# Optimization experiments

Hardware: AMD Instinct MI355X
Metric: run time of the kernel (lower is better)

## Reference

```python
import jax, jax.numpy as jnp
import numpy as np

N_DRUG, N_MICROBE = 1500, 1572
N = N_DRUG + N_MICROBE          # 3072 nodes
F_IN = 1546                     # raw feature dim (fc1: 1546 -> 256)
D0 = 256                        # GCN input dim after fc1
H1 = H2 = 128                   # GCN hidden dims (H1 + H2 = 256)
B = 16384                       # number of (left,right) query pairs


def _sym_norm(A):
    # D^{-1/2} A D^{-1/2} (no self loops), zeros kept for isolated nodes
    deg = A.sum(axis=1)
    d = jnp.where(deg > 0, jax.lax.rsqrt(deg), 0.0)
    return A * d[:, None] * d[None, :]


def _compute_inf(adj, L):
    # dl.compute_inf: L-hop influence = L-th power of sym-normalized adjacency
    An = _sym_norm(adj)
    M = An
    for _ in range(L - 1):
        M = M @ An
    return M


def _gcn_norm(W):
    # GCNConv normalization: add self loops (weight 1), sym-normalize by weighted degree
    Ahat = W + jnp.eye(W.shape[0], dtype=W.dtype)
    deg = Ahat.sum(axis=1)
    d = jnp.where(deg > 0, jax.lax.rsqrt(deg), 0.0)
    return Ahat * d[:, None] * d[None, :]


def _glorot(key, shape):
    return jax.random.normal(key, shape, dtype=jnp.float32) / np.sqrt(shape[0])


def setup_inputs() -> dict:
    key = jax.random.key(0)
    ks = jax.random.split(key, 24)
    u = jax.random.uniform(ks[0], (N, N), dtype=jnp.float32)
    w = jax.random.uniform(ks[1], (N, N), dtype=jnp.float32)
    adj = jnp.where(u < 0.01, w, 0.0)
    adj = jnp.maximum(adj, adj.T)
    X = jax.random.normal(ks[2], (N, F_IN), dtype=jnp.float32)
    left = jax.random.randint(ks[3], (B,), 0, N)
    right = jax.random.randint(ks[4], (B,), 0, N)
    return dict(
        left=left, right=right, X=X, adj=adj, threshold=jnp.float32(1e-4),
        W_fc1=_glorot(ks[5], (F_IN, D0)), b_fc1=jnp.zeros((D0,), jnp.float32),
        Wg1=_glorot(ks[6], (D0, H1)), bg1=jnp.zeros((H1,), jnp.float32),
        Wg2=_glorot(ks[7], (H1, H2)), bg2=jnp.zeros((H2,), jnp.float32),
        Wg3=_glorot(ks[8], (D0, H1)), bg3=jnp.zeros((H1,), jnp.float32),
        Wg4=_glorot(ks[9], (H1, H2)), bg4=jnp.zeros((H2,), jnp.float32),
        Wg5=_glorot(ks[10], (D0, H1)), bg5=jnp.zeros((H1,), jnp.float32),
        Wg6=_glorot(ks[11], (H1, H2)), bg6=jnp.zeros((H2,), jnp.float32),
        cnn_k=jax.random.normal(ks[12], (1, 3, 3, 3), dtype=jnp.float32) * 0.1,
        cnn_b=jnp.zeros((1,), jnp.float32),
        W_a=_glorot(ks[13], (2 * (H1 + H2), 64)), b_a=jnp.zeros((64,), jnp.float32),
        W_b=_glorot(ks[14], (64, 2)), b_b=jnp.zeros((2,), jnp.float32),
    )


def reference(left, right, X, adj, threshold,
              W_fc1, b_fc1, Wg1, bg1, Wg2, bg2, Wg3, bg3, Wg4, bg4,
              Wg5, bg5, Wg6, bg6, cnn_k, cnn_b, W_a, b_a, W_b, b_b):
    X0 = jax.nn.relu(X @ W_fc1 + b_fc1)  # fc1: [N, 1546] -> [N, 256]

    def branch(mask_src, Wa, ba, Wb, bb):
        # dynamically thresholded edges carry the ORIGINAL adj weights
        Wadj = jnp.where(mask_src > threshold, adj, 0.0)
        An = _gcn_norm(Wadj)                       # [N, N]
        e1 = jax.nn.relu(An @ (X0 @ Wa) + ba)      # GCNConv 1
        e2 = jax.nn.relu(An @ (e1 @ Wb) + bb)      # GCNConv 2
        return jnp.concatenate([e1, e2], axis=1)   # [N, 256]

    emb_l2 = branch(_compute_inf(adj, 2), Wg1, bg1, Wg2, bg2)
    emb_l1 = branch(_compute_inf(adj, 1), Wg3, bg3, Wg4, bg4)
    emb_l0 = branch(adj, Wg5, bg5, Wg6, bg6)

    emb = jnp.stack([emb_l0, emb_l1, emb_l2], axis=0)[None]  # [1, 3, N, 256]
    conv = jax.lax.conv_general_dilated(
        emb, cnn_k, window_strides=(1, 1), padding=[(2, 2), (2, 2)],
        rhs_dilation=(2, 2), dimension_numbers=('NCHW', 'OIHW', 'NCHW'))
    emb_all = conv[0, 0] + cnn_b[0]                # [N, 256]

    pair = jnp.concatenate([emb_all[left], emb_all[right]], axis=1)  # [B, 512]
    h = jax.nn.relu(pair @ W_a + b_a)              # dropout is identity at eval
    logits = h @ W_b + b_b                         # [B, 2]
    return logits, emb_all
```

## Files before the change

### kernel.cpp

```cpp
#include <hip/hip_runtime.h>

#define NN 3072
#define FIN 1546
#define KP 1568
#define MAXR 192

#define XS4_BLOCKS (NN * KP / 1024)
#define WSPLIT_BLOCKS (256 * KP / 256)
#define WG_BLOCKS 704
#define CSR_BLOCKS (NN / 4)
#define FC1_BLOCKS (NN / 16 * 4)

typedef __attribute__((ext_vector_type(8))) __bf16 bf16x8;
typedef __attribute__((ext_vector_type(4))) __bf16 bf16x4;
typedef __attribute__((ext_vector_type(4))) float f32x4;

__global__ __launch_bounds__(256) void prep_k(const float* __restrict__ adj,
                                              int* __restrict__ cols, float* __restrict__ vals,
                                              int* __restrict__ cnt, float* __restrict__ dvec,
                                              const float* __restrict__ X,
                                              __bf16* __restrict__ Xh, __bf16* __restrict__ Xl,
                                              const float* __restrict__ W,
                                              __bf16* __restrict__ WhT, __bf16* __restrict__ WlT,
                                              const float* __restrict__ Wga0,
                                              const float* __restrict__ Wga1,
                                              const float* __restrict__ Wga2,
                                              const float* __restrict__ Wgb0,
                                              const float* __restrict__ Wgb1,
                                              const float* __restrict__ Wgb2,
                                              const float* __restrict__ Wa,
                                              __bf16* __restrict__ WgaTh, __bf16* __restrict__ WgaTl,
                                              __bf16* __restrict__ WgbTh, __bf16* __restrict__ WgbTl,
                                              __bf16* __restrict__ WaTh, __bf16* __restrict__ WaTl) {
    int bid = blockIdx.x;
    if (bid < XS4_BLOCKS) {
        int e = (bid * 256 + threadIdx.x) * 4;
        int i = e / KP, c = e - i * KP;
        const float* xr = X + (size_t)i * FIN + c;
        float x0 = (c + 0 < FIN) ? xr[0] : 0.f;
        float x1 = (c + 1 < FIN) ? xr[1] : 0.f;
        float x2 = (c + 2 < FIN) ? xr[2] : 0.f;
        float x3 = (c + 3 < FIN) ? xr[3] : 0.f;
        __bf16 h0 = (__bf16)x0, h1 = (__bf16)x1, h2 = (__bf16)x2, h3 = (__bf16)x3;
        bf16x4 hv = {h0, h1, h2, h3};
        bf16x4 lv = {(__bf16)(x0 - (float)h0), (__bf16)(x1 - (float)h1),
                     (__bf16)(x2 - (float)h2), (__bf16)(x3 - (float)h3)};
        *(bf16x4*)(Xh + e) = hv;
        *(bf16x4*)(Xl + e) = lv;
        return;
    }
    bid -= XS4_BLOCKS;
    if (bid < WSPLIT_BLOCKS) {
        int idx = bid * 256 + threadIdx.x;
        int c = idx / KP, k = idx - c * KP;
        float x = (k < FIN) ? W[(size_t)k * 256 + c] : 0.f;
        __bf16 h = (__bf16)x;
        WhT[idx] = h;
        WlT[idx] = (__bf16)(x - (float)h);
        return;
    }
    bid -= WSPLIT_BLOCKS;
    if (bid < WG_BLOCKS) {
        int idx = bid * 256 + threadIdx.x;
        float x;
        __bf16 *oh, *ol;
        int off;
        if (idx < 98304) {
            int b = idx >> 15, r = idx & 32767;
            int c = r >> 8, k = r & 255;
            const float* Wp = (b == 0) ? Wga0 : (b == 1) ? Wga1 : Wga2;
            x = Wp[k * 128 + c];
            oh = WgaTh; ol = WgaTl; off = idx;
        } else if (idx < 98304 + 49152) {
            int j = idx - 98304;
            int b = j >> 14, r = j & 16383;
            int c = r >> 7, k = r & 127;
            const float* Wp = (b == 0) ? Wgb0 : (b == 1) ? Wgb1 : Wgb2;
            x = Wp[k * 128 + c];
            oh = WgbTh; ol = WgbTl; off = j;
        } else {
            int j = idx - 147456;
            int c = j >> 8, k = j & 255;
            x = (c < 64) ? Wa[(size_t)k * 64 + c] : Wa[(size_t)(256 + k) * 64 + (c - 64)];
            oh = WaTh; ol = WaTl; off = j;
        }
        __bf16 h = (__bf16)x;
        oh[off] = h;
        ol[off] = (__bf16)(x - (float)h);
        return;
    }
    bid -= WG_BLOCKS;
    int i = bid * 4 + (threadIdx.x >> 6);
    int lane = threadIdx.x & 63;
    const float* row = adj + (size_t)i * NN;
    unsigned long long below = (1ull << lane) - 1ull;
    float s = 0.f; int count = 0;
    int base = i * MAXR;
    for (int c0 = 0; c0 < NN; c0 += 256) {
        float4 a4 = *(const float4*)(row + c0 + lane * 4);
        float a[4] = {a4.x, a4.y, a4.z, a4.w};
        s += a[0] + a[1] + a[2] + a[3];
        unsigned long long bal[4];
        #pragma unroll
        for (int u = 0; u < 4; u++) bal[u] = __ballot(a[u] != 0.f);
        int before = 0;
        #pragma unroll
        for (int u = 0; u < 4; u++) before += __popcll(bal[u] & below);
        int local = 0;
        #pragma unroll
        for (int u = 0; u < 4; u++) {
            if (a[u] != 0.f) {
                int pos = count + before + local;
                if (pos < MAXR) { cols[base + pos] = c0 + lane * 4 + u; vals[base + pos] = a[u]; }
                local++;
            }
        }
        int tot = 0;
        #pragma unroll
        for (int u = 0; u < 4; u++) tot += __popcll(bal[u]);
        count += tot;
    }
    for (int off = 32; off; off >>= 1) s += __shfl_xor(s, off);
    if (lane == 0) {
        cnt[i] = count < MAXR ? count : MAXR;
        dvec[i] = (s > 0.f) ? 1.0f / sqrtf(s) : 0.f;
    }
}

__global__ __launch_bounds__(256) void fc1mask_k(const int* __restrict__ cols,
                                                 const float* __restrict__ vals,
                                                 const int* __restrict__ cnt,
                                                 const float* __restrict__ dvec,
                                                 const float* __restrict__ thrp,
                                                 int* __restrict__ mcols,
                                                 float* __restrict__ mvals,
                                                 int* __restrict__ mcnt,
                                                 float* __restrict__ db,
                                                 const __bf16* __restrict__ Xh,
                                                 const __bf16* __restrict__ Xl,
                                                 const __bf16* __restrict__ WhT,
                                                 const __bf16* __restrict__ WlT,
                                                 const float* __restrict__ bias,
                                                 __bf16* __restrict__ X0h,
                                                 __bf16* __restrict__ X0l) {
    __shared__ float ds[NN];
    __shared__ int lcols[MAXR];
    __shared__ float lvals[MAXR];
    __shared__ int lcnt;
    __shared__ float osum;
    int bid = blockIdx.x, tid = threadIdx.x;

    if (bid < FC1_BLOCKS) {
        int rt = bid >> 2;
        int c0 = (bid & 3) * 64;
        int w = tid >> 6, lane = tid & 63;
        int m = lane & 15, q = lane >> 4;
        int r0 = rt * 16;
        int cw = c0 + w * 16;
        const __bf16* xh = Xh + (size_t)(r0 + m) * KP + q * 8;
        const __bf16* xl = Xl + (size_t)(r0 + m) * KP + q * 8;
        const __bf16* bh = WhT + (size_t)(cw + m) * KP + q * 8;
        const __bf16* bl = WlT + (size_t)(cw + m) * KP + q * 8;

        f32x4 acc;
        #pragma unroll
        for (int r = 0; r < 4; r++) acc[r] = 0.f;

        #pragma unroll 7
        for (int ks = 0; ks < KP; ks += 32) {
            bf16x8 ah = *(const bf16x8*)(xh + ks);
            bf16x8 al = *(const bf16x8*)(xl + ks);
            bf16x8 bhv = *(const bf16x8*)(bh + ks);
            bf16x8 blv = *(const bf16x8*)(bl + ks);
            acc = __builtin_amdgcn_mfma_f32_16x16x32_bf16(ah, bhv, acc, 0, 0, 0);
            acc = __builtin_amdgcn_mfma_f32_16x16x32_bf16(ah, blv, acc, 0, 0, 0);
            acc = __builtin_amdgcn_mfma_f32_16x16x32_bf16(al, bhv, acc, 0, 0, 0);
        }
        int col = cw + m;
        float bv = bias[col];
        #pragma unroll
        for (int r = 0; r < 4; r++) {
            int row = r0 + q * 4 + r;
            float s = fmaxf(acc[r] + bv, 0.f);
            __bf16 h = (__bf16)s;
            X0h[(size_t)row * 256 + col] = h;
            X0l[(size_t)row * 256 + col] = (__bf16)(s - (float)h);
        }
        return;
    }

    int t = bid - FC1_BLOCKS;
    int mode, i;
    if (t < NN)          { mode = 2; i = t; }
    else if (t < 2 * NN) { mode = 0; i = t - NN; }
    else                 { mode = 1; i = t - 2 * NN; }

    mcols += (size_t)mode * NN * MAXR;
    mvals += (size_t)mode * NN * MAXR;
    mcnt  += (size_t)mode * NN;
    db    += (size_t)mode * NN;
    int ni = cnt[i], base = i * MAXR;
    float thr = *thrp;
    float di = dvec[i];

    if (mode < 2) {
        if (tid == 0) lcnt = 0;
        __syncthreads();
        float s = 0.f;
        if (tid < ni) {
            int j = cols[base + tid];
            float a = vals[base + tid];
            float m = (mode == 0) ? a : a * di * dvec[j];
            if (m > thr) {
                int p = atomicAdd(&lcnt, 1);
                mcols[base + p] = j;
                mvals[base + p] = a;
                s = a;
            }
        }
        ds[tid] = s; __syncthreads();
        for (int off = 128; off; off >>= 1) {
            if (tid < off) ds[tid] += ds[tid + off];
            __syncthreads();
        }
        if (tid == 0) {
            mcnt[i] = lcnt;
            db[i] = 1.0f / sqrtf(ds[0] + 1.0f);
        }
        return;
    }

    if (tid == 0) { osum = 0.f; lcnt = 0; }
    for (int j = tid; j < NN; j += 256) ds[j] = 0.f;
    __syncthreads();
    for (int t2 = tid; t2 < ni; t2 += 256) {
        int j = cols[base + t2];
        float a = vals[base + t2];
        lcols[t2] = j; lvals[t2] = a;
        ds[j] = a * dvec[j] * dvec[j];
    }
    __syncthreads();
    int lane = tid & 63, wv = tid >> 6;
    int sub = lane & 15, dg = lane >> 4;
    for (int o = wv * 4 + dg; o < ni; o += 16) {
        int j = lcols[o];
        int nj = cnt[j], bj = j * MAXR;
        float dot = 0.f;
        for (int t2 = sub; t2 < nj; t2 += 16)
            dot += vals[bj + t2] * ds[cols[bj + t2]];
        #pragma unroll
        for (int off = 8; off; off >>= 1) dot += __shfl_xor(dot, off);
        if (sub == 0 && di * dvec[j] * dot > thr) {
            int p = atomicAdd(&lcnt, 1);
            mcols[base + p] = j;
            mvals[base + p] = lvals[o];
            atomicAdd(&osum, lvals[o]);
        }
    }
    __syncthreads();
    if (tid == 0) {
        mcnt[i] = lcnt;
        db[i] = 1.0f / sqrtf(osum + 1.0f);
    }
}

__global__ __launch_bounds__(256) void gemm3m_k(const __bf16* __restrict__ Ah,
                                                const __bf16* __restrict__ Al,
                                                int aplane, int K,
                                                const __bf16* __restrict__ Bh,
                                                const __bf16* __restrict__ Bl,
                                                float* __restrict__ out) {
    int tid = threadIdx.x;
    int w = tid >> 6, lane = tid & 63;
    int m = lane & 15, q = lane >> 4;
    int i0 = blockIdx.x * 64, c0 = blockIdx.y * 64;
    int z = blockIdx.z;
    int rowA = i0 + w * 16 + m;
    const __bf16* ah = Ah + (size_t)z * aplane + (size_t)rowA * K + q * 8;
    const __bf16* al = Al + (size_t)z * aplane + (size_t)rowA * K + q * 8;
    const __bf16* bh0 = Bh + (size_t)z * 128 * K + (size_t)(c0 + m) * K + q * 8;
    const __bf16* bl0 = Bl + (size_t)z * 128 * K + (size_t)(c0 + m) * K + q * 8;

    f32x4 acc[4];
    #pragma unroll
    for (int ct = 0; ct < 4; ct++)
        #pragma unroll
        for (int r = 0; r < 4; r++) acc[ct][r] = 0.f;

    for (int ks = 0; ks < K; ks += 32) {
        bf16x8 a_h = *(const bf16x8*)(ah + ks);
        bf16x8 a_l = *(const bf16x8*)(al + ks);
        #pragma unroll
        for (int ct = 0; ct < 4; ct++) {
            bf16x8 b_h = *(const bf16x8*)(bh0 + (size_t)ct * 16 * K + ks);
            bf16x8 b_l = *(const bf16x8*)(bl0 + (size_t)ct * 16 * K + ks);
            acc[ct] = __builtin_amdgcn_mfma_f32_16x16x32_bf16(a_h, b_h, acc[ct], 0, 0, 0);
            acc[ct] = __builtin_amdgcn_mfma_f32_16x16x32_bf16(a_h, b_l, acc[ct], 0, 0, 0);
            acc[ct] = __builtin_amdgcn_mfma_f32_16x16x32_bf16(a_l, b_h, acc[ct], 0, 0, 0);
        }
    }
    float* outp = out + (size_t)z * NN * 128;
    int rowBase = i0 + w * 16 + q * 4;
    #pragma unroll
    for (int ct = 0; ct < 4; ct++) {
        int col = c0 + ct * 16 + m;
        #pragma unroll
        for (int r = 0; r < 4; r++)
            outp[(size_t)(rowBase + r) * 128 + col] = acc[ct][r];
    }
}

__global__ __launch_bounds__(256) void spmm3_k(const int* __restrict__ mcols,
                                               const float* __restrict__ mvals,
                                               const int* __restrict__ mcnt,
                                               const float* __restrict__ db,
                                               const float* __restrict__ Xin,
                                               const float* __restrict__ bias0,
                                               const float* __restrict__ bias1,
                                               const float* __restrict__ bias2,
                                               __bf16* __restrict__ outAh,
                                               __bf16* __restrict__ outAl,
                                               float* __restrict__ embf, int coff) {
    __shared__ float lcoef[MAXR];
    __shared__ int lj[MAXR];
    __shared__ float4 part[8][32];
    int i = blockIdx.x, tid = threadIdx.x, b = blockIdx.y;
    mcols += (size_t)b * NN * MAXR;
    mvals += (size_t)b * NN * MAXR;
    mcnt  += (size_t)b * NN;
    db    += (size_t)b * NN;
    const float* Xb = Xin + (size_t)b * NN * 128;
    const float* bias = (b == 0) ? bias0 : (b == 1) ? bias1 : bias2;
    float dbi = db[i];
    int n = mcnt[i], base = i * MAXR;
    if (tid < n) {
        int j = mcols[base + tid];
        lj[tid] = j;
        lcoef[tid] = mvals[base + tid] * dbi * db[j];
    }
    __syncthreads();
    int g = tid >> 5, c4 = (tid & 31) << 2;
    float4 acc = make_float4(0.f, 0.f, 0.f, 0.f);
    float4 acc2 = make_float4(0.f, 0.f, 0.f, 0.f);
    if (g == 0) {
        float4 x = *(const float4*)&Xb[(size_t)i * 128 + c4];
        float d2 = dbi * dbi;
        acc = make_float4(d2 * x.x, d2 * x.y, d2 * x.z, d2 * x.w);
    }
    int t = g;
    for (; t + 8 < n; t += 16) {
        float cf0 = lcoef[t];
        float4 x0 = *(const float4*)&Xb[(size_t)lj[t] * 128 + c4];
        float cf1 = lcoef[t + 8];
        float4 x1 = *(const float4*)&Xb[(size_t)lj[t + 8] * 128 + c4];
        acc.x += cf0 * x0.x; acc.y += cf0 * x0.y; acc.z += cf0 * x0.z; acc.w += cf0 * x0.w;
        acc2.x += cf1 * x1.x; acc2.y += cf1 * x1.y; acc2.z += cf1 * x1.z; acc2.w += cf1 * x1.w;
    }
    if (t < n) {
        float cf = lcoef[t];
        float4 x = *(const float4*)&Xb[(size_t)lj[t] * 128 + c4];
        acc.x += cf * x.x; acc.y += cf * x.y; acc.z += cf * x.z; acc.w += cf * x.w;
    }
    acc.x += acc2.x; acc.y += acc2.y; acc.z += acc2.z; acc.w += acc2.w;
    part[g][tid & 31] = acc;
    __syncthreads();
    if (tid < 32) {
        float4 s = part[0][tid];
        #pragma unroll
        for (int gg = 1; gg < 8; gg++) {
            float4 t4 = part[gg][tid];
            s.x += t4.x; s.y += t4.y; s.z += t4.z; s.w += t4.w;
        }
        int cc = tid << 2;
        float4 bv = *(const float4*)&bias[cc];
        s.x = fmaxf(s.x + bv.x, 0.f); s.y = fmaxf(s.y + bv.y, 0.f);
        s.z = fmaxf(s.z + bv.z, 0.f); s.w = fmaxf(s.w + bv.w, 0.f);
        if (outAh) {
            __bf16 h0 = (__bf16)s.x, h1 = (__bf16)s.y, h2 = (__bf16)s.z, h3 = (__bf16)s.w;
            bf16x4 hv = {h0, h1, h2, h3};
            bf16x4 lv = {(__bf16)(s.x - (float)h0), (__bf16)(s.y - (float)h1),
                         (__bf16)(s.z - (float)h2), (__bf16)(s.w - (float)h3)};
            *(bf16x4*)(outAh + ((size_t)b * NN + i) * 128 + cc) = hv;
            *(bf16x4*)(outAl + ((size_t)b * NN + i) * 128 + cc) = lv;
        }
        *(float4*)&embf[((size_t)b * NN + i) * 256 + coff + cc] = s;
    }
}

__global__ __launch_bounds__(256) void conv3f_k(const float* __restrict__ emb,
                                                const float* __restrict__ ck,
                                                const float* __restrict__ cb,
                                                float* __restrict__ outf,
                                                __bf16* __restrict__ embh,
                                                __bf16* __restrict__ embl) {
    __shared__ float rows[3][3][256];
    int n = blockIdx.x, c = threadIdx.x;
    #pragma unroll
    for (int i = 0; i < 3; i++)
        #pragma unroll
        for (int kh = 0; kh < 3; kh++) {
            int nn2 = n + 2 * kh - 2;
            rows[i][kh][c] = (nn2 >= 0 && nn2 < NN) ? emb[((size_t)i * NN + nn2) * 256 + c] : 0.f;
        }
    __syncthreads();
    float s = cb[0];
    #pragma unroll
    for (int i = 0; i < 3; i++)
        #pragma unroll
        for (int kh = 0; kh < 3; kh++)
            #pragma unroll
            for (int kw = 0; kw < 3; kw++) {
                int cc = c + 2 * kw - 2;
                if (cc >= 0 && cc < 256)
                    s += rows[i][kh][cc] * ck[(i * 3 + kh) * 3 + kw];
            }
    size_t idx = (size_t)n * 256 + c;
    outf[idx] = s;
    __bf16 h = (__bf16)s;
    embh[idx] = h;
    embl[idx] = (__bf16)(s - (float)h);
}

__global__ __launch_bounds__(256) void gemmuvm_k(const __bf16* __restrict__ Ah,
                                                 const __bf16* __restrict__ Al,
                                                 const __bf16* __restrict__ Bh,
                                                 const __bf16* __restrict__ Bl,
                                                 float* __restrict__ uvp) {
    int tid = threadIdx.x;
    int w = tid >> 6, lane = tid & 63;
    int m = lane & 15, q = lane >> 4;
    int i0 = blockIdx.x * 64, c0 = blockIdx.y * 64;
    int rowA = i0 + w * 16 + m;
    const __bf16* ah = Ah + (size_t)rowA * 256 + q * 8;
    const __bf16* al = Al + (size_t)rowA * 256 + q * 8;
    const __bf16* bh0 = Bh + (size_t)(c0 + m) * 256 + q * 8;
    const __bf16* bl0 = Bl + (size_t)(c0 + m) * 256 + q * 8;

    f32x4 acc[4];
    #pragma unroll
    for (int ct = 0; ct < 4; ct++)
        #pragma unroll
        for (int r = 0; r < 4; r++) acc[ct][r] = 0.f;

    for (int ks = 0; ks < 256; ks += 32) {
        bf16x8 a_h = *(const bf16x8*)(ah + ks);
        bf16x8 a_l = *(const bf16x8*)(al + ks);
        #pragma unroll
        for (int ct = 0; ct < 4; ct++) {
            bf16x8 b_h = *(const bf16x8*)(bh0 + (size_t)ct * 16 * 256 + ks);
            bf16x8 b_l = *(const bf16x8*)(bl0 + (size_t)ct * 16 * 256 + ks);
            acc[ct] = __builtin_amdgcn_mfma_f32_16x16x32_bf16(a_h, b_h, acc[ct], 0, 0, 0);
            acc[ct] = __builtin_amdgcn_mfma_f32_16x16x32_bf16(a_h, b_l, acc[ct], 0, 0, 0);
            acc[ct] = __builtin_amdgcn_mfma_f32_16x16x32_bf16(a_l, b_h, acc[ct], 0, 0, 0);
        }
    }
    int rowBase = i0 + w * 16 + q * 4;
    #pragma unroll
    for (int ct = 0; ct < 4; ct++) {
        int col = c0 + ct * 16 + m;
        #pragma unroll
        for (int r = 0; r < 4; r++)
            uvp[(size_t)(rowBase + r) * 128 + col] = acc[ct][r];
    }
}

__global__ __launch_bounds__(256) void pairuv_k(const int* __restrict__ left,
                                                const int* __restrict__ right,
                                                const float* __restrict__ uvp,
                                                const float* __restrict__ ba,
                                                const float* __restrict__ Wb,
                                                const float* __restrict__ bb,
                                                float* __restrict__ out) {
    int tid = threadIdx.x;
    int w = tid >> 6, c = tid & 63;
    int base = blockIdx.x * 16 + w * 4;
    float bac = ba[c];
    float w0 = Wb[c * 2], w1 = Wb[c * 2 + 1];
    float b0 = bb[0], b1 = bb[1];
    #pragma unroll
    for (int pp = 0; pp < 4; pp++) {
        int row = base + pp;
        int l = left[row], r = right[row];
        float h = uvp[(size_t)l * 128 + c] + uvp[(size_t)r * 128 + 64 + c] + bac;
        h = fmaxf(h, 0.f);
        float s0 = h * w0, s1 = h * w1;
        for (int off = 32; off; off >>= 1) {
            s0 += __shfl_xor(s0, off);
            s1 += __shfl_xor(s1, off);
        }
        if (c == 0) {
            out[row * 2]     = s0 + b0;
            out[row * 2 + 1] = s1 + b1;
        }
    }
}

extern "C" void kernel_launch(void* const* d_in, const int* in_sizes, int n_in,
                              void* d_out, int out_size, void* d_ws, size_t ws_size,
                              hipStream_t stream) {
    const int* left  = (const int*)d_in[0];
    const int* right = (const int*)d_in[1];
    const float* X    = (const float*)d_in[2];
    const float* adj  = (const float*)d_in[3];
    const float* thr  = (const float*)d_in[4];
    const float* Wfc1 = (const float*)d_in[5];
    const float* bfc1 = (const float*)d_in[6];
    const float* Wga[3] = { (const float*)d_in[15], (const float*)d_in[11], (const float*)d_in[7] };
    const float* bga[3] = { (const float*)d_in[16], (const float*)d_in[12], (const float*)d_in[8] };
    const float* Wgb[3] = { (const float*)d_in[17], (const float*)d_in[13], (const float*)d_in[9] };
    const float* bgb[3] = { (const float*)d_in[18], (const float*)d_in[14], (const float*)d_in[10] };
    const float* cnnk = (const float*)d_in[19];
    const float* cnnb = (const float*)d_in[20];
    const float* Wa_  = (const float*)d_in[21];
    const float* ba_  = (const float*)d_in[22];
    const float* Wb_  = (const float*)d_in[23];
    const float* bb_  = (const float*)d_in[24];

    char* p = (char*)d_ws;
    auto take = [&](size_t n) { char* q = p; p += (n + 255) & ~(size_t)255; return q; };
    float* dvec = (float*)take(NN * 4);
    float* db3  = (float*)take((size_t)3 * NN * 4);
    int*   cnt  = (int*)take(NN * 4);
    int*   mcnt3 = (int*)take((size_t)3 * NN * 4);
    int*   cols = (int*)take((size_t)NN * MAXR * 4);
    float* vals = (float*)take((size_t)NN * MAXR * 4);
    int*   mcols3 = (int*)take((size_t)3 * NN * MAXR * 4);
    float* mvals3 = (float*)take((size_t)3 * NN * MAXR * 4);
    __bf16* X0h  = (__bf16*)take((size_t)NN * 256 * 2);
    __bf16* X0l  = (__bf16*)take((size_t)NN * 256 * 2);
    float* XWall = (float*)take((size_t)3 * NN * 128 * 4);
    __bf16* e1h  = (__bf16*)take((size_t)3 * NN * 128 * 2);
    __bf16* e1l  = (__bf16*)take((size_t)3 * NN * 128 * 2);
    float* HW2all= (float*)take((size_t)3 * NN * 128 * 4);
    float* embf  = (float*)take((size_t)3 * NN * 256 * 4);
    __bf16* Xh   = (__bf16*)take((size_t)NN * KP * 2);
    __bf16* Xl   = (__bf16*)take((size_t)NN * KP * 2);
    __bf16* WhT  = (__bf16*)take((size_t)256 * KP * 2);
    __bf16* WlT  = (__bf16*)take((size_t)256 * KP * 2);
    __bf16* WgaTh = (__bf16*)take((size_t)3 * 128 * 256 * 2);
    __bf16* WgaTl = (__bf16*)take((size_t)3 * 128 * 256 * 2);
    __bf16* WgbTh = (__bf16*)take((size_t)3 * 128 * 128 * 2);
    __bf16* WgbTl = (__bf16*)take((size_t)3 * 128 * 128 * 2);
    __bf16* WaTh  = (__bf16*)take((size_t)128 * 256 * 2);
    __bf16* WaTl  = (__bf16*)take((size_t)128 * 256 * 2);
    __bf16* embh  = (__bf16*)take((size_t)NN * 256 * 2);
    __bf16* embl  = (__bf16*)take((size_t)NN * 256 * 2);
    float* uvp   = (float*)take((size_t)NN * 128 * 4);

    float* out_logits = (float*)d_out;
    float* out_emb = out_logits + 32768;

    prep_k<<<XS4_BLOCKS + WSPLIT_BLOCKS + WG_BLOCKS + CSR_BLOCKS, 256, 0, stream>>>(
        adj, cols, vals, cnt, dvec, X, Xh, Xl, Wfc1, WhT, WlT,
        Wga[0], Wga[1], Wga[2], Wgb[0], Wgb[1], Wgb[2], Wa_,
        WgaTh, WgaTl, WgbTh, WgbTl, WaTh, WaTl);

    fc1mask_k<<<FC1_BLOCKS + 3 * NN, 256, 0, stream>>>(cols, vals, cnt, dvec, thr,
                                                       mcols3, mvals3, mcnt3, db3,
                                                       Xh, Xl, WhT, WlT, bfc1, X0h, X0l);

    gemm3m_k<<<dim3(NN / 64, 2, 3), 256, 0, stream>>>(X0h, X0l, 0, 256, WgaTh, WgaTl, XWall);
    spmm3_k<<<dim3(NN, 3), 256, 0, stream>>>(mcols3, mvals3, mcnt3, db3, XWall,
                                             bga[0], bga[1], bga[2], e1h, e1l, embf, 0);
    gemm3m_k<<<dim3(NN / 64, 2, 3), 256, 0, stream>>>(e1h, e1l, NN * 128, 128, WgbTh, WgbTl, HW2all);
    spmm3_k<<<dim3(NN, 3), 256, 0, stream>>>(mcols3, mvals3, mcnt3, db3, HW2all,
                                             bgb[0], bgb[1], bgb[2], (__bf16*)0, (__bf16*)0, embf, 128);

    conv3f_k<<<NN, 256, 0, stream>>>(embf, cnnk, cnnb, out_emb, embh, embl);
    gemmuvm_k<<<dim3(NN / 64, 2), 256, 0, stream>>>(embh, embl, WaTh, WaTl, uvp);
    pairuv_k<<<16384 / 16, 256, 0, stream>>>(left, right, uvp, ba_, Wb_, bb_, out_logits);
}
```

Measured before the change: 303.5 us.

## Fuse all pipeline stages into one persistent cooperative kernel with grid syncs

Replaces nine separate kernel launches with a single cooperative persistent kernel. Each former kernel becomes a device function processed in a grid-stride loop, and grid-wide barriers separate the stages. This removes per-launch overhead and inter-kernel gaps. In exchange, every stage must run within a fixed occupancy-limited grid and a unified shared-memory footprint, and the grid barriers carry their own cost.

```diff
diff --git a/kernel.cpp b/kernel.cpp
--- a/kernel.cpp
+++ b/kernel.cpp
@@ -1,4 +1,6 @@
 #include <hip/hip_runtime.h>
+#include <hip/hip_cooperative_groups.h>
+namespace cg = cooperative_groups;
 
 #define NN 3072
 #define FIN 1546
@@ -9,34 +11,35 @@
 #define WSPLIT_BLOCKS (256 * KP / 256)
 #define WG_BLOCKS 704
 #define CSR_BLOCKS (NN / 4)
-#define FC1_BLOCKS (NN / 16 * 4)
+#define PREP_UNITS (XS4_BLOCKS + WSPLIT_BLOCKS + WG_BLOCKS + CSR_BLOCKS)
+#define FC1_UNITS (NN / 16 * 4)
+#define P1_UNITS (FC1_UNITS + 3 * NN)
 
 typedef __attribute__((ext_vector_type(8))) __bf16 bf16x8;
 typedef __attribute__((ext_vector_type(4))) __bf16 bf16x4;
 typedef __attribute__((ext_vector_type(4))) float f32x4;
 
-__global__ __launch_bounds__(256) void prep_k(const float* __restrict__ adj,
-                                              int* __restrict__ cols, float* __restrict__ vals,
-                                              int* __restrict__ cnt, float* __restrict__ dvec,
-                                              const float* __restrict__ X,
-                                              __bf16* __restrict__ Xh, __bf16* __restrict__ Xl,
-                                              const float* __restrict__ W,
-                                              __bf16* __restrict__ WhT, __bf16* __restrict__ WlT,
-                                              const float* __restrict__ Wga0,
-                                              const float* __restrict__ Wga1,
-                                              const float* __restrict__ Wga2,
-                                              const float* __restrict__ Wgb0,
-                                              const float* __restrict__ Wgb1,
-                                              const float* __restrict__ Wgb2,
-                                              const float* __restrict__ Wa,
-                                              __bf16* __restrict__ WgaTh, __bf16* __restrict__ WgaTl,
-                                              __bf16* __restrict__ WgbTh, __bf16* __restrict__ WgbTl,
-                                              __bf16* __restrict__ WaTh, __bf16* __restrict__ WaTl) {
-    int bid = blockIdx.x;
+struct MegaArgs {
+    const float *adj, *X, *Wfc1, *bfc1, *thr;
+    const float *Wga0, *Wga1, *Wga2, *Wgb0, *Wgb1, *Wgb2, *Wa;
+    const float *bga0, *bga1, *bga2, *bgb0, *bgb1, *bgb2;
+    const float *cnnk, *cnnb, *ba, *Wb, *bb;
+    const int *left, *right;
+    int *cols; float *vals; int *cnt; float *dvec;
+    int *mcols; float *mvals; int *mcnt; float *db;
+    __bf16 *Xh, *Xl, *WhT, *WlT;
+    __bf16 *WgaTh, *WgaTl, *WgbTh, *WgbTl, *WaTh, *WaTl;
+    __bf16 *X0h, *X0l;
+    float *XWall; __bf16 *e1h, *e1l; float *HW2all; float *embf;
+    __bf16 *embh, *embl; float *uvp;
+    float *out_logits, *out_emb;
+};
+
+__device__ __forceinline__ void prep_unit(const MegaArgs& A, int bid, int tid) {
     if (bid < XS4_BLOCKS) {
-        int e = (bid * 256 + threadIdx.x) * 4;
+        int e = (bid * 256 + tid) * 4;
         int i = e / KP, c = e - i * KP;
-        const float* xr = X + (size_t)i * FIN + c;
+        const float* xr = A.X + (size_t)i * FIN + c;
         float x0 = (c + 0 < FIN) ? xr[0] : 0.f;
         float x1 = (c + 1 < FIN) ? xr[1] : 0.f;
         float x2 = (c + 2 < FIN) ? xr[2] : 0.f;
@@ -45,54 +48,54 @@
         bf16x4 hv = {h0, h1, h2, h3};
         bf16x4 lv = {(__bf16)(x0 - (float)h0), (__bf16)(x1 - (float)h1),
                      (__bf16)(x2 - (float)h2), (__bf16)(x3 - (float)h3)};
-        *(bf16x4*)(Xh + e) = hv;
-        *(bf16x4*)(Xl + e) = lv;
+        *(bf16x4*)(A.Xh + e) = hv;
+        *(bf16x4*)(A.Xl + e) = lv;
         return;
     }
-    bid -= XS4_BLOCKS;
-    if (bid < WSPLIT_BLOCKS) {
-        int idx = bid * 256 + threadIdx.x;
+    int b2 = bid - XS4_BLOCKS;
+    if (b2 < WSPLIT_BLOCKS) {
+        int idx = b2 * 256 + tid;
         int c = idx / KP, k = idx - c * KP;
-        float x = (k < FIN) ? W[(size_t)k * 256 + c] : 0.f;
+        float x = (k < FIN) ? A.Wfc1[(size_t)k * 256 + c] : 0.f;
         __bf16 h = (__bf16)x;
-        WhT[idx] = h;
-        WlT[idx] = (__bf16)(x - (float)h);
+        A.WhT[idx] = h;
+        A.WlT[idx] = (__bf16)(x - (float)h);
         return;
     }
-    bid -= WSPLIT_BLOCKS;
-    if (bid < WG_BLOCKS) {
-        int idx = bid * 256 + threadIdx.x;
+    b2 -= WSPLIT_BLOCKS;
+    if (b2 < WG_BLOCKS) {
+        int idx = b2 * 256 + tid;
         float x;
         __bf16 *oh, *ol;
         int off;
         if (idx < 98304) {
             int b = idx >> 15, r = idx & 32767;
             int c = r >> 8, k = r & 255;
-            const float* Wp = (b == 0) ? Wga0 : (b == 1) ? Wga1 : Wga2;
+            const float* Wp = (b == 0) ? A.Wga0 : (b == 1) ? A.Wga1 : A.Wga2;
             x = Wp[k * 128 + c];
-            oh = WgaTh; ol = WgaTl; off = idx;
+            oh = A.WgaTh; ol = A.WgaTl; off = idx;
         } else if (idx < 98304 + 49152) {
             int j = idx - 98304;
             int b = j >> 14, r = j & 16383;
             int c = r >> 7, k = r & 127;
-            const float* Wp = (b == 0) ? Wgb0 : (b == 1) ? Wgb1 : Wgb2;
+            const float* Wp = (b == 0) ? A.Wgb0 : (b == 1) ? A.Wgb1 : A.Wgb2;
             x = Wp[k * 128 + c];
-            oh = WgbTh; ol = WgbTl; off = j;
+            oh = A.WgbTh; ol = A.WgbTl; off = j;
         } else {
             int j = idx - 147456;
             int c = j >> 8, k = j & 255;
-            x = (c < 64) ? Wa[(size_t)k * 64 + c] : Wa[(size_t)(256 + k) * 64 + (c - 64)];
-            oh = WaTh; ol = WaTl; off = j;
+            x = (c < 64) ? A.Wa[(size_t)k * 64 + c] : A.Wa[(size_t)(256 + k) * 64 + (c - 64)];
+            oh = A.WaTh; ol = A.WaTl; off = j;
         }
         __bf16 h = (__bf16)x;
         oh[off] = h;
         ol[off] = (__bf16)(x - (float)h);
         return;
     }
-    bid -= WG_BLOCKS;
-    int i = bid * 4 + (threadIdx.x >> 6);
-    int lane = threadIdx.x & 63;
-    const float* row = adj + (size_t)i * NN;
+    b2 -= WG_BLOCKS;
+    int i = b2 * 4 + (tid >> 6);
+    int lane = tid & 63;
+    const float* row = A.adj + (size_t)i * NN;
     unsigned long long below = (1ull << lane) - 1ull;
     float s = 0.f; int count = 0;
     int base = i * MAXR;
@@ -111,7 +114,7 @@
         for (int u = 0; u < 4; u++) {
             if (a[u] != 0.f) {
                 int pos = count + before + local;
-                if (pos < MAXR) { cols[base + pos] = c0 + lane * 4 + u; vals[base + pos] = a[u]; }
+                if (pos < MAXR) { A.cols[base + pos] = c0 + lane * 4 + u; A.vals[base + pos] = a[u]; }
                 local++;
             }
         }
@@ -122,97 +125,78 @@
     }
     for (int off = 32; off; off >>= 1) s += __shfl_xor(s, off);
     if (lane == 0) {
-        cnt[i] = count < MAXR ? count : MAXR;
-        dvec[i] = (s > 0.f) ? 1.0f / sqrtf(s) : 0.f;
-    }
-}
-
-__global__ __launch_bounds__(256) void fc1mask_k(const int* __restrict__ cols,
-                                                 const float* __restrict__ vals,
-                                                 const int* __restrict__ cnt,
-                                                 const float* __restrict__ dvec,
-                                                 const float* __restrict__ thrp,
-                                                 int* __restrict__ mcols,
-                                                 float* __restrict__ mvals,
-                                                 int* __restrict__ mcnt,
-                                                 float* __restrict__ db,
-                                                 const __bf16* __restrict__ Xh,
-                                                 const __bf16* __restrict__ Xl,
-                                                 const __bf16* __restrict__ WhT,
-                                                 const __bf16* __restrict__ WlT,
-                                                 const float* __restrict__ bias,
-                                                 __bf16* __restrict__ X0h,
-                                                 __bf16* __restrict__ X0l) {
-    __shared__ float ds[NN];
-    __shared__ int lcols[MAXR];
-    __shared__ float lvals[MAXR];
-    __shared__ int lcnt;
-    __shared__ float osum;
-    int bid = blockIdx.x, tid = threadIdx.x;
-
-    if (bid < FC1_BLOCKS) {
-        int rt = bid >> 2;
-        int c0 = (bid & 3) * 64;
-        int w = tid >> 6, lane = tid & 63;
-        int m = lane & 15, q = lane >> 4;
-        int r0 = rt * 16;
-        int cw = c0 + w * 16;
-        const __bf16* xh = Xh + (size_t)(r0 + m) * KP + q * 8;
-        const __bf16* xl = Xl + (size_t)(r0 + m) * KP + q * 8;
-        const __bf16* bh = WhT + (size_t)(cw + m) * KP + q * 8;
-        const __bf16* bl = WlT + (size_t)(cw + m) * KP + q * 8;
-
-        f32x4 acc;
-        #pragma unroll
-        for (int r = 0; r < 4; r++) acc[r] = 0.f;
-
-        #pragma unroll 7
-        for (int ks = 0; ks < KP; ks += 32) {
-            bf16x8 ah = *(const bf16x8*)(xh + ks);
-            bf16x8 al = *(const bf16x8*)(xl + ks);
-            bf16x8 bhv = *(const bf16x8*)(bh + ks);
-            bf16x8 blv = *(const bf16x8*)(bl + ks);
-            acc = __builtin_amdgcn_mfma_f32_16x16x32_bf16(ah, bhv, acc, 0, 0, 0);
-            acc = __builtin_amdgcn_mfma_f32_16x16x32_bf16(ah, blv, acc, 0, 0, 0);
-            acc = __builtin_amdgcn_mfma_f32_16x16x32_bf16(al, bhv, acc, 0, 0, 0);
-        }
-        int col = cw + m;
-        float bv = bias[col];
-        #pragma unroll
-        for (int r = 0; r < 4; r++) {
-            int row = r0 + q * 4 + r;
-            float s = fmaxf(acc[r] + bv, 0.f);
-            __bf16 h = (__bf16)s;
-            X0h[(size_t)row * 256 + col] = h;
-            X0l[(size_t)row * 256 + col] = (__bf16)(s - (float)h);
-        }
-        return;
-    }
-
-    int t = bid - FC1_BLOCKS;
+        A.cnt[i] = count < MAXR ? count : MAXR;
+        A.dvec[i] = (s > 0.f) ? 1.0f / sqrtf(s) : 0.f;
+    }
+}
+
+__device__ __forceinline__ void fc1_unit(const MegaArgs& A, int u, int tid) {
+    int rt = u >> 2;
+    int c0 = (u & 3) * 64;
+    int w = tid >> 6, lane = tid & 63;
+    int m = lane & 15, q = lane >> 4;
+    int r0 = rt * 16;
+    int cw = c0 + w * 16;
+    const __bf16* xh = A.Xh + (size_t)(r0 + m) * KP + q * 8;
+    const __bf16* xl = A.Xl + (size_t)(r0 + m) * KP + q * 8;
+    const __bf16* bh = A.WhT + (size_t)(cw + m) * KP + q * 8;
+    const __bf16* bl = A.WlT + (size_t)(cw + m) * KP + q * 8;
+
+    f32x4 acc;
+    #pragma unroll
+    for (int r = 0; r < 4; r++) acc[r] = 0.f;
+
+    #pragma unroll 7
+    for (int ks = 0; ks < KP; ks += 32) {
+        bf16x8 ah = *(const bf16x8*)(xh + ks);
+        bf16x8 al = *(const bf16x8*)(xl + ks);
+        bf16x8 bhv = *(const bf16x8*)(bh + ks);
+        bf16x8 blv = *(const bf16x8*)(bl + ks);
+        acc = __builtin_amdgcn_mfma_f32_16x16x32_bf16(ah, bhv, acc, 0, 0, 0);
+        acc = __builtin_amdgcn_mfma_f32_16x16x32_bf16(ah, blv, acc, 0, 0, 0);
+        acc = __builtin_amdgcn_mfma_f32_16x16x32_bf16(al, bhv, acc, 0, 0, 0);
+    }
+    int col = cw + m;
+    float bv = A.bfc1[col];
+    #pragma unroll
+    for (int r = 0; r < 4; r++) {
+        int row = r0 + q * 4 + r;
+        float s = fmaxf(acc[r] + bv, 0.f);
+        __bf16 h = (__bf16)s;
+        A.X0h[(size_t)row * 256 + col] = h;
+        A.X0l[(size_t)row * 256 + col] = (__bf16)(s - (float)h);
+    }
+}
+
+__device__ __forceinline__ void mask_unit(const MegaArgs& A, int t, int tid, char* smem) {
+    float* ds    = (float*)smem;
+    int*   lcols = (int*)(smem + 12288);
+    float* lvals = (float*)(smem + 13056);
+    int*   lcnt  = (int*)(smem + 13824);
+    float* osum  = (float*)(smem + 13828);
     int mode, i;
     if (t < NN)          { mode = 2; i = t; }
     else if (t < 2 * NN) { mode = 0; i = t - NN; }
     else                 { mode = 1; i = t - 2 * NN; }
 
-    mcols += (size_t)mode * NN * MAXR;
-    mvals += (size_t)mode * NN * MAXR;
-    mcnt  += (size_t)mode * NN;
-    db    += (size_t)mode * NN;
-    int ni = cnt[i], base = i * MAXR;
-    float thr = *thrp;
-    float di = dvec[i];
+    int* mcols = A.mcols + (size_t)mode * NN * MAXR;
+    float* mvals = A.mvals + (size_t)mode * NN * MAXR;
+    int* mcnt = A.mcnt + (size_t)mode * NN;
+    float* db = A.db + (size_t)mode * NN;
+    int ni = A.cnt[i], base = i * MAXR;
+    float thr = *A.thr;
+    float di = A.dvec[i];
 
     if (mode < 2) {
-        if (tid == 0) lcnt = 0;
+        if (tid == 0) *lcnt = 0;
         __syncthreads();
         float s = 0.f;
         if (tid < ni) {
-            int j = cols[base + tid];
-            float a = vals[base + tid];
-            float m = (mode == 0) ? a : a * di * dvec[j];
-            if (m > thr) {
-                int p = atomicAdd(&lcnt, 1);
+            int j = A.cols[base + tid];
+            float a = A.vals[base + tid];
+            float mv = (mode == 0) ? a : a * di * A.dvec[j];
+            if (mv > thr) {
+                int p = atomicAdd(lcnt, 1);
                 mcols[base + p] = j;
                 mvals[base + p] = a;
                 s = a;
@@ -224,62 +208,61 @@
             __syncthreads();
         }
         if (tid == 0) {
-            mcnt[i] = lcnt;
+            mcnt[i] = *lcnt;
             db[i] = 1.0f / sqrtf(ds[0] + 1.0f);
         }
         return;
     }
 
-    if (tid == 0) { osum = 0.f; lcnt = 0; }
+    if (tid == 0) { *osum = 0.f; *lcnt = 0; }
     for (int j = tid; j < NN; j += 256) ds[j] = 0.f;
     __syncthreads();
     for (int t2 = tid; t2 < ni; t2 += 256) {
-        int j = cols[base + t2];
-        float a = vals[base + t2];
+        int j = A.cols[base + t2];
+        float a = A.vals[base + t2];
         lcols[t2] = j; lvals[t2] = a;
-        ds[j] = a * dvec[j] * dvec[j];
+        ds[j] = a * A.dvec[j] * A.dvec[j];
     }
     __syncthreads();
     int lane = tid & 63, wv = tid >> 6;
     int sub = lane & 15, dg = lane >> 4;
     for (int o = wv * 4 + dg; o < ni; o += 16) {
         int j = lcols[o];
-        int nj = cnt[j], bj = j * MAXR;
+        int nj = A.cnt[j], bj = j * MAXR;
         float dot = 0.f;
         for (int t2 = sub; t2 < nj; t2 += 16)
-            dot += vals[bj + t2] * ds[cols[bj + t2]];
+            dot += A.vals[bj + t2] * ds[A.cols[bj + t2]];
         #pragma unroll
         for (int off = 8; off; off >>= 1) dot += __shfl_xor(dot, off);
-        if (sub == 0 && di * dvec[j] * dot > thr) {
-            int p = atomicAdd(&lcnt, 1);
+        if (sub == 0 && di * A.dvec[j] * dot > thr) {
+            int p = atomicAdd(lcnt, 1);
             mcols[base + p] = j;
             mvals[base + p] = lvals[o];
-            atomicAdd(&osum, lvals[o]);
+            atomicAdd(osum, lvals[o]);
         }
     }
     __syncthreads();
     if (tid == 0) {
-        mcnt[i] = lcnt;
-        db[i] = 1.0f / sqrtf(osum + 1.0f);
-    }
-}
-
-__global__ __launch_bounds__(256) void gemm3m_k(const __bf16* __restrict__ Ah,
-                                                const __bf16* __restrict__ Al,
-                                                int aplane, int K,
-                                                const __bf16* __restrict__ Bh,
-                                                const __bf16* __restrict__ Bl,
-                                                float* __restrict__ out) {
-    int tid = threadIdx.x;
+        mcnt[i] = *lcnt;
+        db[i] = 1.0f / sqrtf(*osum + 1.0f);
+    }
+}
+
+__device__ __forceinline__ void gemm_unit(const __bf16* __restrict__ Ah,
+                                          const __bf16* __restrict__ Al,
+                                          int aplane, int K,
+                                          const __bf16* __restrict__ Bh,
+                                          const __bf16* __restrict__ Bl,
+                                          float* __restrict__ out,
+                                          int bx, int by, int bz, int tid) {
     int w = tid >> 6, lane = tid & 63;
     int m = lane & 15, q = lane >> 4;
-    int i0 = blockIdx.x * 64, c0 = blockIdx.y * 64;
-    int z = blockIdx.z;
+    int i0 = bx * 64, c0 = by * 64;
     int rowA = i0 + w * 16 + m;
-    const __bf16* ah = Ah + (size_t)z * aplane + (size_t)rowA * K + q * 8;
-    const __bf16* al = Al + (size_t)z * aplane + (size_t)rowA * K + q * 8;
-    const __bf16* bh0 = Bh + (size_t)z * 128 * K + (size_t)(c0 + m) * K + q * 8;
-    const __bf16* bl0 = Bl + (size_t)z * 128 * K + (size_t)(c0 + m) * K + q * 8;
+    const __bf16* ah = Ah + (size_t)bz * aplane + (size_t)rowA * K + q * 8;
+    const __bf16* al = Al + (size_t)bz * aplane + (size_t)rowA * K + q * 8;
+    const __bf16* bh0 = Bh + (size_t)bz * 128 * K + (size_t)(c0 + m) * K + q * 8;
+    const __bf16* bl0 = Bl + (size_t)bz * 128 * K + (size_t)(c0 + m) * K + q * 8;
 
     f32x4 acc[4];
     #pragma unroll
@@ -299,7 +282,7 @@
             acc[ct] = __builtin_amdgcn_mfma_f32_16x16x32_bf16(a_l, b_h, acc[ct], 0, 0, 0);
         }
     }
-    float* outp = out + (size_t)z * NN * 128;
+    float* outp = out + (size_t)bz * NN * 128;
     int rowBase = i0 + w * 16 + q * 4;
     #pragma unroll
     for (int ct = 0; ct < 4; ct++) {
@@ -310,25 +293,21 @@
     }
 }
 
-__global__ __launch_bounds__(256) void spmm3_k(const int* __restrict__ mcols,
-                                               const float* __restrict__ mvals,
-                                               const int* __restrict__ mcnt,
-                                               const float* __restrict__ db,
-                                               const float* __restrict__ Xin,
-                                               const float* __restrict__ bias0,
-                                               const float* __restrict__ bias1,
-                                               const float* __restrict__ bias2,
-                                               __bf16* __restrict__ outAh,
-                                               __bf16* __restrict__ outAl,
-                                               float* __restrict__ embf, int coff) {
-    __shared__ float lcoef[MAXR];
-    __shared__ int lj[MAXR];
-    __shared__ float4 part[8][32];
-    int i = blockIdx.x, tid = threadIdx.x, b = blockIdx.y;
-    mcols += (size_t)b * NN * MAXR;
-    mvals += (size_t)b * NN * MAXR;
-    mcnt  += (size_t)b * NN;
-    db    += (size_t)b * NN;
+__device__ __forceinline__ void spmm_unit(const MegaArgs& A, int b, int i,
+                                          const float* __restrict__ Xin,
+                                          const float* __restrict__ bias0,
+                                          const float* __restrict__ bias1,
+                                          const float* __restrict__ bias2,
+                                          __bf16* __restrict__ outAh,
+                                          __bf16* __restrict__ outAl,
+                                          int coff, int tid, char* smem) {
+    float* lcoef = (float*)smem;
+    int*   lj    = (int*)(smem + 768);
+    float4* part = (float4*)(smem + 1536);
+    const int* mcols = A.mcols + (size_t)b * NN * MAXR;
+    const float* mvals = A.mvals + (size_t)b * NN * MAXR;
+    const int* mcnt = A.mcnt + (size_t)b * NN;
+    const float* db = A.db + (size_t)b * NN;
     const float* Xb = Xin + (size_t)b * NN * 128;
     const float* bias = (b == 0) ? bias0 : (b == 1) ? bias1 : bias2;
     float dbi = db[i];
@@ -362,13 +341,13 @@
         acc.x += cf * x.x; acc.y += cf * x.y; acc.z += cf * x.z; acc.w += cf * x.w;
     }
     acc.x += acc2.x; acc.y += acc2.y; acc.z += acc2.z; acc.w += acc2.w;
-    part[g][tid & 31] = acc;
+    part[g * 32 + (tid & 31)] = acc;
     __syncthreads();
     if (tid < 32) {
-        float4 s = part[0][tid];
+        float4 s = part[tid];
         #pragma unroll
         for (int gg = 1; gg < 8; gg++) {
-            float4 t4 = part[gg][tid];
+            float4 t4 = part[gg * 32 + tid];
             s.x += t4.x; s.y += t4.y; s.z += t4.z; s.w += t4.w;
         }
         int cc = tid << 2;
@@ -383,27 +362,23 @@
             *(bf16x4*)(outAh + ((size_t)b * NN + i) * 128 + cc) = hv;
             *(bf16x4*)(outAl + ((size_t)b * NN + i) * 128 + cc) = lv;
         }
-        *(float4*)&embf[((size_t)b * NN + i) * 256 + coff + cc] = s;
-    }
-}
-
-__global__ __launch_bounds__(256) void conv3f_k(const float* __restrict__ emb,
-                                                const float* __restrict__ ck,
-                                                const float* __restrict__ cb,
-                                                float* __restrict__ outf,
-                                                __bf16* __restrict__ embh,
-                                                __bf16* __restrict__ embl) {
-    __shared__ float rows[3][3][256];
-    int n = blockIdx.x, c = threadIdx.x;
+        *(float4*)&A.embf[((size_t)b * NN + i) * 256 + coff + cc] = s;
+    }
+}
+
+__device__ __forceinline__ void conv_unit(const MegaArgs& A, int n, int tid, char* smem) {
+    float* rows = (float*)smem;
+    int c = tid;
     #pragma unroll
     for (int i = 0; i < 3; i++)
         #pragma unroll
         for (int kh = 0; kh < 3; kh++) {
             int nn2 = n + 2 * kh - 2;
-            rows[i][kh][c] = (nn2 >= 0 && nn2 < NN) ? emb[((size_t)i * NN + nn2) * 256 + c] : 0.f;
+            rows[(i * 3 + kh) * 256 + c] =
+                (nn2 >= 0 && nn2 < NN) ? A.embf[((size_t)i * NN + nn2) * 256 + c] : 0.f;
         }
     __syncthreads();
-    float s = cb[0];
+    float s = A.cnnb[0];
     #pragma unroll
     for (int i = 0; i < 3; i++)
         #pragma unroll
@@ -412,29 +387,24 @@
             for (int kw = 0; kw < 3; kw++) {
                 int cc = c + 2 * kw - 2;
                 if (cc >= 0 && cc < 256)
-                    s += rows[i][kh][cc] * ck[(i * 3 + kh) * 3 + kw];
+                    s += rows[(i * 3 + kh) * 256 + cc] * A.cnnk[(i * 3 + kh) * 3 + kw];
             }
     size_t idx = (size_t)n * 256 + c;
-    outf[idx] = s;
+    A.out_emb[idx] = s;
     __bf16 h = (__bf16)s;
-    embh[idx] = h;
-    embl[idx] = (__bf16)(s - (float)h);
-}
-
-__global__ __launch_bounds__(256) void gemmuvm_k(const __bf16* __restrict__ Ah,
-                                                 const __bf16* __restrict__ Al,
-                                                 const __bf16* __restrict__ Bh,
-                                                 const __bf16* __restrict__ Bl,
-                                                 float* __restrict__ uvp) {
-    int tid = threadIdx.x;
+    A.embh[idx] = h;
+    A.embl[idx] = (__bf16)(s - (float)h);
+}
+
+__device__ __forceinline__ void uv_unit(const MegaArgs& A, int bx, int by, int tid) {
     int w = tid >> 6, lane = tid & 63;
     int m = lane & 15, q = lane >> 4;
-    int i0 = blockIdx.x * 64, c0 = blockIdx.y * 64;
+    int i0 = bx * 64, c0 = by * 64;
     int rowA = i0 + w * 16 + m;
-    const __bf16* ah = Ah + (size_t)rowA * 256 + q * 8;
-    const __bf16* al = Al + (size_t)rowA * 256 + q * 8;
-    const __bf16* bh0 = Bh + (size_t)(c0 + m) * 256 + q * 8;
-    const __bf16* bl0 = Bl + (size_t)(c0 + m) * 256 + q * 8;
+    const __bf16* ah = A.embh + (size_t)rowA * 256 + q * 8;
+    const __bf16* al = A.embl + (size_t)rowA * 256 + q * 8;
+    const __bf16* bh0 = A.WaTh + (size_t)(c0 + m) * 256 + q * 8;
+    const __bf16* bl0 = A.WaTl + (size_t)(c0 + m) * 256 + q * 8;
 
     f32x4 acc[4];
     #pragma unroll
@@ -460,28 +430,21 @@
         int col = c0 + ct * 16 + m;
         #pragma unroll
         for (int r = 0; r < 4; r++)
-            uvp[(size_t)(rowBase + r) * 128 + col] = acc[ct][r];
-    }
-}
-
-__global__ __launch_bounds__(256) void pairuv_k(const int* __restrict__ left,
-                                                const int* __restrict__ right,
-                                                const float* __restrict__ uvp,
-                                                const float* __restrict__ ba,
-                                                const float* __restrict__ Wb,
-                                                const float* __restrict__ bb,
-                                                float* __restrict__ out) {
-    int tid = threadIdx.x;
+            A.uvp[(size_t)(rowBase + r) * 128 + col] = acc[ct][r];
+    }
+}
+
+__device__ __forceinline__ void pair_unit(const MegaArgs& A, int u, int tid) {
     int w = tid >> 6, c = tid & 63;
-    int base = blockIdx.x * 16 + w * 4;
-    float bac = ba[c];
-    float w0 = Wb[c * 2], w1 = Wb[c * 2 + 1];
-    float b0 = bb[0], b1 = bb[1];
+    int base = u * 16 + w * 4;
+    float bac = A.ba[c];
+    float w0 = A.Wb[c * 2], w1 = A.Wb[c * 2 + 1];
+    float b0 = A.bb[0], b1 = A.bb[1];
     #pragma unroll
     for (int pp = 0; pp < 4; pp++) {
         int row = base + pp;
-        int l = left[row], r = right[row];
-        float h = uvp[(size_t)l * 128 + c] + uvp[(size_t)r * 128 + 64 + c] + bac;
+        int l = A.left[row], r = A.right[row];
+        float h = A.uvp[(size_t)l * 128 + c] + A.uvp[(size_t)r * 128 + 64 + c] + bac;
         h = fmaxf(h, 0.f);
         float s0 = h * w0, s1 = h * w1;
         for (int off = 32; off; off >>= 1) {
@@ -489,10 +452,67 @@
             s1 += __shfl_xor(s1, off);
         }
         if (c == 0) {
-            out[row * 2]     = s0 + b0;
-            out[row * 2 + 1] = s1 + b1;
-        }
-    }
+            A.out_logits[row * 2]     = s0 + b0;
+            A.out_logits[row * 2 + 1] = s1 + b1;
+        }
+    }
+}
+
+__global__ __launch_bounds__(256, 4) void mega_k(MegaArgs A) {
+    cg::grid_group gg = cg::this_grid();
+    __shared__ __align__(16) char smem[13856];
+    int tid = threadIdx.x;
+    int gb = gridDim.x;
+
+    for (int u = blockIdx.x; u < PREP_UNITS; u += gb) prep_unit(A, u, tid);
+    gg.sync();
+
+    for (int u = blockIdx.x; u < P1_UNITS; u += gb) {
+        if (u < FC1_UNITS) fc1_unit(A, u, tid);
+        else mask_unit(A, u - FC1_UNITS, tid, smem);
+        __syncthreads();
+    }
+    gg.sync();
+
+    for (int u = blockIdx.x; u < 288; u += gb) {
+        int bx = u % 48, by = (u / 48) & 1, bz = u / 96;
+        gemm_unit(A.X0h, A.X0l, 0, 256, A.WgaTh, A.WgaTl, A.XWall, bx, by, bz, tid);
+    }
+    gg.sync();
+
+    for (int u = blockIdx.x; u < 3 * NN; u += gb) {
+        int i = u % NN, b = u / NN;
+        spmm_unit(A, b, i, A.XWall, A.bga0, A.bga1, A.bga2, A.e1h, A.e1l, 0, tid, smem);
+        __syncthreads();
+    }
+    gg.sync();
+
+    for (int u = blockIdx.x; u < 288; u += gb) {
+        int bx = u % 48, by = (u / 48) & 1, bz = u / 96;
+        gemm_unit(A.e1h, A.e1l, NN * 128, 128, A.WgbTh, A.WgbTl, A.HW2all, bx, by, bz, tid);
+    }
+    gg.sync();
+
+    for (int u = blockIdx.x; u < 3 * NN; u += gb) {
+        int i = u % NN, b = u / NN;
+        spmm_unit(A, b, i, A.HW2all, A.bgb0, A.bgb1, A.bgb2, (__bf16*)0, (__bf16*)0, 128, tid, smem);
+        __syncthreads();
+    }
+    gg.sync();
+
+    for (int u = blockIdx.x; u < NN; u += gb) {
+        conv_unit(A, u, tid, smem);
+        __syncthreads();
+    }
+    gg.sync();
+
+    for (int u = blockIdx.x; u < 96; u += gb) {
+        int bx = u % 48, by = u / 48;
+        uv_unit(A, bx, by, tid);
+    }
+    gg.sync();
+
+    for (int u = blockIdx.x; u < 1024; u += gb) pair_unit(A, u, tid);
 }
 
 extern "C" void kernel_launch(void* const* d_in, const int* in_sizes, int n_in,
@@ -550,23 +570,33 @@
     float* out_logits = (float*)d_out;
     float* out_emb = out_logits + 32768;
 
-    prep_k<<<XS4_BLOCKS + WSPLIT_BLOCKS + WG_BLOCKS + CSR_BLOCKS, 256, 0, stream>>>(
-        adj, cols, vals, cnt, dvec, X, Xh, Xl, Wfc1, WhT, WlT,
-        Wga[0], Wga[1], Wga[2], Wgb[0], Wgb[1], Wgb[2], Wa_,
-        WgaTh, WgaTl, WgbTh, WgbTl, WaTh, WaTl);
-
-    fc1mask_k<<<FC1_BLOCKS + 3 * NN, 256, 0, stream>>>(cols, vals, cnt, dvec, thr,
-                                                       mcols3, mvals3, mcnt3, db3,
-                                                       Xh, Xl, WhT, WlT, bfc1, X0h, X0l);
-
-    gemm3m_k<<<dim3(NN / 64, 2, 3), 256, 0, stream>>>(X0h, X0l, 0, 256, WgaTh, WgaTl, XWall);
-    spmm3_k<<<dim3(NN, 3), 256, 0, stream>>>(mcols3, mvals3, mcnt3, db3, XWall,
-                                             bga[0], bga[1], bga[2], e1h, e1l, embf, 0);
-    gemm3m_k<<<dim3(NN / 64, 2, 3), 256, 0, stream>>>(e1h, e1l, NN * 128, 128, WgbTh, WgbTl, HW2all);
-    spmm3_k<<<dim3(NN, 3), 256, 0, stream>>>(mcols3, mvals3, mcnt3, db3, HW2all,
-                                             bgb[0], bgb[1], bgb[2], (__bf16*)0, (__bf16*)0, embf, 128);
-
-    conv3f_k<<<NN, 256, 0, stream>>>(embf, cnnk, cnnb, out_emb, embh, embl);
-    gemmuvm_k<<<dim3(NN / 64, 2), 256, 0, stream>>>(embh, embl, WaTh, WaTl, uvp);
-    pairuv_k<<<16384 / 16, 256, 0, stream>>>(left, right, uvp, ba_, Wb_, bb_, out_logits);
-}
+    MegaArgs a;
+    a.adj = adj; a.X = X; a.Wfc1 = Wfc1; a.bfc1 = bfc1; a.thr = thr;
+    a.Wga0 = Wga[0]; a.Wga1 = Wga[1]; a.Wga2 = Wga[2];
+    a.Wgb0 = Wgb[0]; a.Wgb1 = Wgb[1]; a.Wgb2 = Wgb[2]; a.Wa = Wa_;
+    a.bga0 = bga[0]; a.bga1 = bga[1]; a.bga2 = bga[2];
+    a.bgb0 = bgb[0]; a.bgb1 = bgb[1]; a.bgb2 = bgb[2];
+    a.cnnk = cnnk; a.cnnb = cnnb; a.ba = ba_; a.Wb = Wb_; a.bb = bb_;
+    a.left = left; a.right = right;
+    a.cols = cols; a.vals = vals; a.cnt = cnt; a.dvec = dvec;
+    a.mcols = mcols3; a.mvals = mvals3; a.mcnt = mcnt3; a.db = db3;
+    a.Xh = Xh; a.Xl = Xl; a.WhT = WhT; a.WlT = WlT;
+    a.WgaTh = WgaTh; a.WgaTl = WgaTl; a.WgbTh = WgbTh; a.WgbTl = WgbTl;
+    a.WaTh = WaTh; a.WaTl = WaTl;
+    a.X0h = X0h; a.X0l = X0l;
+    a.XWall = XWall; a.e1h = e1h; a.e1l = e1l; a.HW2all = HW2all; a.embf = embf;
+    a.embh = embh; a.embl = embl; a.uvp = uvp;
+    a.out_logits = out_logits; a.out_emb = out_emb;
+
+    static int megaGrid = 0;
+    if (megaGrid == 0) {
+        int occ = 0;
+        hipOccupancyMaxActiveBlocksPerMultiprocessor(&occ, mega_k, 256, 0);
+        if (occ < 1) occ = 1;
+        if (occ > 8) occ = 8;
+        megaGrid = occ * 256;
+    }
+
+    void* kargs[] = { (void*)&a };
+    hipLaunchCooperativeKernel(mega_k, dim3(megaGrid), dim3(256), kargs, 0, stream);
+}
```

After: 981.4 us. 3.23x slower.
